# Performance work log

Hardware: AMD Instinct MI355X
Metric: run time of the kernel (lower is better)

Reference implementation:

```python
import jax, jax.numpy as jnp
import numpy as np

H = W = 240

def setup_inputs() -> dict:
    key = jax.random.key(0)
    k1, k2, k3 = jax.random.split(key, 3)
    B = 256
    T2_Gen = jax.random.normal(k1, (B, 1, H, W), dtype=jnp.float32)
    underT2_K = jax.random.normal(k2, (B, 2, H, W), dtype=jnp.float32)
    # k-space sampling mask (soft in [0,1); original uses a fixed undersampling mask)
    A = jax.random.uniform(k3, (H, W), dtype=jnp.float32)
    return {"T2_Gen": T2_Gen, "underT2_K": underT2_K, "A": A}

def reference(T2_Gen, underT2_K, A):
    # x2: [B, H, W]
    x2 = T2_Gen.reshape(-1, H, W)
    # batched 2D FFT over the last two axes (replaces the per-slice numpy loop)
    x2_k = jnp.fft.fft2(x2)  # complex64
    # undersampled k-space as complex: real = channel 0, imag = channel 1
    y_k = underT2_K[:, 0, :, :] + 1j * underT2_K[:, 1, :, :]
    z_k = (1.0 - A) * x2_k + y_k
    z = jnp.abs(jnp.fft.ifft2(z_k))  # [B, H, W] real
    return z.reshape(-1, 1, H, W)
```

## Files before the change

### kernel.cpp

```cpp
#include <hip/hip_runtime.h>
#include <math.h>

#define HW 240
#define PITCH 241
#define IMG_PIX (HW*HW)

__device__ __forceinline__ float2 cmul(float2 a, float2 b){
    return make_float2(a.x*b.x - a.y*b.y, a.x*b.y + a.y*b.x);
}
__device__ __forceinline__ float2 cadd(float2 a, float2 b){
    return make_float2(a.x+b.x, a.y+b.y);
}
__device__ __forceinline__ float2 csub(float2 a, float2 b){
    return make_float2(a.x-b.x, a.y-b.y);
}

template<int SIGN>
__device__ __forceinline__ void dft15(const float2* x, float2* X){
    const float S = (float)SIGN;
    const float s3 = 0.8660254037844387f;
    float2 y[5][3];
    #pragma unroll
    for (int n2 = 0; n2 < 5; ++n2){
        float2 a0 = x[n2], a1 = x[5+n2], a2 = x[10+n2];
        float2 t = cadd(a1, a2);
        float2 u = csub(a1, a2);
        float2 m = make_float2(a0.x - 0.5f*t.x, a0.y - 0.5f*t.y);
        float sx = S * s3;
        float2 s = make_float2(-sx*u.y, sx*u.x);
        y[n2][0] = cadd(a0, t);
        y[n2][1] = cadd(m, s);
        y[n2][2] = csub(m, s);
    }
    const float C15[9] = {1.f, 0.9135454576426009f, 0.6691306063588582f, 0.30901699437494745f,
                          -0.10452846326765346f, -0.5f, -0.8090169943749475f,
                          -0.9781476007338057f, -0.9781476007338057f};
    const float S15[9] = {0.f, 0.4067366430758004f, 0.7431448254773942f, 0.9510565162951535f,
                          0.9945218953682733f, 0.8660254037844387f, 0.5877852522924731f,
                          0.20791169081775931f, -0.20791169081775931f};
    #pragma unroll
    for (int n2 = 1; n2 < 5; ++n2){
        #pragma unroll
        for (int k1 = 1; k1 < 3; ++k1){
            const int e = n2*k1;
            y[n2][k1] = cmul(y[n2][k1], make_float2(C15[e], S*S15[e]));
        }
    }
    const float c1 = 0.30901699437494745f, s1 = 0.9510565162951535f;
    const float c2 = -0.8090169943749475f, s2 = 0.5877852522924731f;
    #pragma unroll
    for (int k1 = 0; k1 < 3; ++k1){
        float2 x0 = y[0][k1], x1 = y[1][k1], x2 = y[2][k1], x3 = y[3][k1], x4 = y[4][k1];
        float2 t1 = cadd(x1, x4), t3 = csub(x1, x4);
        float2 t2 = cadd(x2, x3), t4 = csub(x2, x3);
        X[k1] = make_float2(x0.x + t1.x + t2.x, x0.y + t1.y + t2.y);
        float2 u1 = make_float2(x0.x + c1*t1.x + c2*t2.x, x0.y + c1*t1.y + c2*t2.y);
        float2 u2 = make_float2(x0.x + c2*t1.x + c1*t2.x, x0.y + c2*t1.y + c1*t2.y);
        float2 v1 = make_float2(S*(s1*t3.x + s2*t4.x), S*(s1*t3.y + s2*t4.y));
        float2 v2 = make_float2(S*(s2*t3.x - s1*t4.x), S*(s2*t3.y - s1*t4.y));
        X[k1+3]  = make_float2(u1.x - v1.y, u1.y + v1.x);
        X[k1+12] = make_float2(u1.x + v1.y, u1.y - v1.x);
        X[k1+6]  = make_float2(u2.x - v2.y, u2.y + v2.x);
        X[k1+9]  = make_float2(u2.x + v2.y, u2.y - v2.x);
    }
}

template<int SIGN>
__device__ __forceinline__ void dft16(const float2* x, float2* X){
    const float S = (float)SIGN;
    float2 y[4][4];
    #pragma unroll
    for (int n2 = 0; n2 < 4; ++n2){
        float2 a0 = x[n2], a1 = x[4+n2], a2 = x[8+n2], a3 = x[12+n2];
        float2 t0 = cadd(a0,a2), t1 = csub(a0,a2);
        float2 t2 = cadd(a1,a3), t3 = csub(a1,a3);
        float2 it3 = make_float2(-S*t3.y, S*t3.x);
        y[n2][0] = cadd(t0,t2);
        y[n2][2] = csub(t0,t2);
        y[n2][1] = cadd(t1,it3);
        y[n2][3] = csub(t1,it3);
    }
    const float C16[10] = {1.f, 0.9238795325112867f, 0.7071067811865476f, 0.3826834323650898f,
                           0.f, -0.3826834323650898f, -0.7071067811865476f, -0.9238795325112867f,
                           -1.f, -0.9238795325112867f};
    const float S16[10] = {0.f, 0.3826834323650898f, 0.7071067811865476f, 0.9238795325112867f,
                           1.f, 0.9238795325112867f, 0.7071067811865476f, 0.3826834323650898f,
                           0.f, -0.3826834323650898f};
    #pragma unroll
    for (int n2 = 1; n2 < 4; ++n2){
        #pragma unroll
        for (int k1 = 1; k1 < 4; ++k1){
            const int e = n2*k1;
            y[n2][k1] = cmul(y[n2][k1], make_float2(C16[e], S*S16[e]));
        }
    }
    #pragma unroll
    for (int k1 = 0; k1 < 4; ++k1){
        float2 a0 = y[0][k1], a1 = y[1][k1], a2 = y[2][k1], a3 = y[3][k1];
        float2 t0 = cadd(a0,a2), t1 = csub(a0,a2);
        float2 t2 = cadd(a1,a3), t3 = csub(a1,a3);
        float2 it3 = make_float2(-S*t3.y, S*t3.x);
        X[k1]    = cadd(t0,t2);
        X[k1+8]  = csub(t0,t2);
        X[k1+4]  = cadd(t1,it3);
        X[k1+12] = csub(t1,it3);
    }
}

template<int SIGN>
__device__ void fft240(float2 (*sm)[PITCH], float2* v, int rl, int b){
    const float TWOPI = 6.28318530717958647692f;
    float2 Y[15];
    dft15<SIGN>(v, Y);
    float2 step, tw = make_float2(1.0f, 0.0f);
    {
        float ang = (float)SIGN * TWOPI * (float)b * (1.0f/240.0f);
        __sincosf(ang, &step.y, &step.x);
    }
    #pragma unroll
    for (int d = 0; d < 15; ++d){
        sm[rl][b*15 + d] = cmul(Y[d], tw);
        tw = cmul(tw, step);
    }
    __syncthreads();

    float2 Z[16];
    if (b < 15){
        #pragma unroll
        for (int bb = 0; bb < 16; ++bb) Z[bb] = sm[rl][bb*15 + b];
    }
    __syncthreads();
    if (b < 15){
        float2 XX[16];
        dft16<SIGN>(Z, XX);
        #pragma unroll
        for (int m = 0; m < 16; ++m) sm[rl][15*m + b] = XX[m];
    }
    __syncthreads();
}

__global__ __launch_bounds__(256) void passA_rowfft(const float* __restrict__ x,
                                                    float2* __restrict__ out){
    __shared__ float2 sm[16][PITCH];
    int g = blockIdx.x, img = g / 15, row0 = (g % 15) * 16;
    int tid = threadIdx.x, rl = tid >> 4, b = tid & 15;
    const float* src = x + (size_t)img * IMG_PIX + (size_t)(row0 + rl) * HW + b;
    float2 v[15];
    #pragma unroll
    for (int a = 0; a < 15; ++a) v[a] = make_float2(src[16*a], 0.0f);
    fft240<-1>(sm, v, rl, b);
    float2* dst = out + (size_t)img * IMG_PIX;
    #pragma unroll
    for (int j = 0; j < 15; ++j){
        int k  = j*16 + rl;
        dst[(size_t)k * HW + row0 + b] = sm[b][k];
    }
}

__global__ __launch_bounds__(256) void passB_col_dc_icol(const float2* __restrict__ in,
                                                         const float* __restrict__ under,
                                                         const float* __restrict__ Am,
                                                         float2* __restrict__ out){
    __shared__ float2 sm[16][PITCH];
    int g = blockIdx.x, img = g / 15, row0 = (g % 15) * 16;
    int tid = threadIdx.x, rl = tid >> 4, b = tid & 15;
    const float2* src = in + (size_t)img * IMG_PIX + (size_t)(row0 + rl) * HW + b;
    float2 v[15];
    #pragma unroll
    for (int a = 0; a < 15; ++a) v[a] = src[16*a];
    fft240<-1>(sm, v, rl, b);

    const float* y0 = under + (size_t)img * (2*IMG_PIX);
    const float* y1 = y0 + IMG_PIX;
    #pragma unroll
    for (int j = 0; j < 15; ++j){
        int kh = j*16 + rl;
        size_t p = (size_t)kh * HW + row0 + b;
        float s = 1.0f - Am[p];
        float2 X = sm[b][kh];
        sm[b][kh] = make_float2(s * X.x + y0[p], s * X.y + y1[p]);
    }
    __syncthreads();
    #pragma unroll
    for (int a = 0; a < 15; ++a) v[a] = sm[rl][16*a + b];
    __syncthreads();
    fft240<+1>(sm, v, rl, b);

    float2* dst = out + (size_t)img * IMG_PIX;
    #pragma unroll
    for (int j = 0; j < 15; ++j){
        int h = j*16 + rl;
        dst[(size_t)h * HW + row0 + b] = sm[b][h];
    }
}

__global__ __launch_bounds__(256) void passC_irow_abs(const float2* __restrict__ in,
                                                      float* __restrict__ out){
    __shared__ float2 sm[16][PITCH];
    int g = blockIdx.x, img = g / 15, row0 = (g % 15) * 16;
    int tid = threadIdx.x, rl = tid >> 4, b = tid & 15;
    const float2* src = in + (size_t)img * IMG_PIX + (size_t)(row0 + rl) * HW + b;
    float2 v[15];
    #pragma unroll
    for (int a = 0; a < 15; ++a) v[a] = src[16*a];
    fft240<+1>(sm, v, rl, b);
    float* dst = out + (size_t)img * IMG_PIX;
    const float scale = 1.0f / (float)IMG_PIX;
    #pragma unroll
    for (int j = 0; j < 15; ++j){
        int w = j*16 + b;
        float2 X = sm[rl][w];
        dst[(size_t)(row0 + rl) * HW + w] = sqrtf(X.x*X.x + X.y*X.y) * scale;
    }
}

extern "C" void kernel_launch(void* const* d_in, const int* in_sizes, int n_in,
                              void* d_out, int out_size, void* d_ws, size_t ws_size,
                              hipStream_t stream){
    const float* T2   = (const float*)d_in[0];
    const float* U    = (const float*)d_in[1];
    const float* Am   = (const float*)d_in[2];
    float* out        = (float*)d_out;

    const int B = 256;
    float2* s1 = (float2*)d_ws;
    float2* s2 = s1 + (size_t)B * IMG_PIX;

    dim3 grid(B * 15), block(256);
    passA_rowfft     <<<grid, block, 0, stream>>>(T2, s1);
    passB_col_dc_icol<<<grid, block, 0, stream>>>(s1, U, Am, s2);
    passC_irow_abs   <<<grid, block, 0, stream>>>(s2, out);
}
```

Before: 313.4 us.

## Store FFT intermediates as half2 in tiled layout with coalesced staging

The complex intermediates between the three FFT passes are now stored as fp16 half2 instead of float2, which halves intermediate global traffic. They are written in a column-tile-major layout so each block reads and writes one contiguous tile, and global loads and stores go through shared memory to stay coalesced. Normalization is split into a 1/240 factor applied after the column pass and again at the end, which keeps fp16 values in range. The risk is accuracy loss from fp16 rounding of FFT values, plus extra shared-memory staging and barriers.

Measured after the change: 283.6 us. 9.5% less time.

```diff
diff --git a/kernel.cpp b/kernel.cpp
--- a/kernel.cpp
+++ b/kernel.cpp
@@ -1,9 +1,12 @@
 #include <hip/hip_runtime.h>
+#include <hip/hip_fp16.h>
 #include <math.h>
 
 #define HW 240
 #define PITCH 241
 #define IMG_PIX (HW*HW)
+#define NB 15
+#define TILE_ELEMS (240*16)
 
 __device__ __forceinline__ float2 cmul(float2 a, float2 b){
     return make_float2(a.x*b.x - a.y*b.y, a.x*b.y + a.y*b.x);
@@ -14,6 +17,8 @@
 __device__ __forceinline__ float2 csub(float2 a, float2 b){
     return make_float2(a.x-b.x, a.y-b.y);
 }
+__device__ __forceinline__ __half2 f2h(float2 a){ return __floats2half2_rn(a.x, a.y); }
+__device__ __forceinline__ float2 h2f(__half2 h){ return make_float2(__low2float(h), __high2float(h)); }
 
 template<int SIGN>
 __device__ __forceinline__ void dft15(const float2* x, float2* X){
@@ -140,34 +145,49 @@
 }
 
 __global__ __launch_bounds__(256) void passA_rowfft(const float* __restrict__ x,
-                                                    float2* __restrict__ out){
+                                                    __half2* __restrict__ out){
     __shared__ float2 sm[16][PITCH];
-    int g = blockIdx.x, img = g / 15, row0 = (g % 15) * 16;
+    float* smf = (float*)sm;
+    int g = blockIdx.x, img = g / NB, h0 = (g % NB) * 16;
     int tid = threadIdx.x, rl = tid >> 4, b = tid & 15;
-    const float* src = x + (size_t)img * IMG_PIX + (size_t)(row0 + rl) * HW + b;
+    const float* src = x + (size_t)img * IMG_PIX + (size_t)h0 * HW;
+    #pragma unroll
+    for (int j = 0; j < 15; ++j){
+        int f = j*256 + tid;
+        smf[(f/HW)*(2*PITCH) + (f%HW)] = src[f];
+    }
+    __syncthreads();
     float2 v[15];
     #pragma unroll
-    for (int a = 0; a < 15; ++a) v[a] = make_float2(src[16*a], 0.0f);
+    for (int a = 0; a < 15; ++a) v[a] = make_float2(smf[rl*(2*PITCH) + 16*a + b], 0.0f);
+    __syncthreads();
     fft240<-1>(sm, v, rl, b);
-    float2* dst = out + (size_t)img * IMG_PIX;
-    #pragma unroll
-    for (int j = 0; j < 15; ++j){
-        int k  = j*16 + rl;
-        dst[(size_t)k * HW + row0 + b] = sm[b][k];
-    }
-}
-
-__global__ __launch_bounds__(256) void passB_col_dc_icol(const float2* __restrict__ in,
+    int hl = rl, kwin = b;
+    #pragma unroll
+    for (int kb = 0; kb < NB; ++kb){
+        float2 val = sm[hl][kb*16 + kwin];
+        out[((size_t)(img*NB + kb)*HW + h0 + hl)*16 + kwin] = f2h(val);
+    }
+}
+
+__global__ __launch_bounds__(256) void passB_col_dc_icol(const __half2* __restrict__ in,
                                                          const float* __restrict__ under,
                                                          const float* __restrict__ Am,
-                                                         float2* __restrict__ out){
+                                                         __half2* __restrict__ out){
     __shared__ float2 sm[16][PITCH];
-    int g = blockIdx.x, img = g / 15, row0 = (g % 15) * 16;
+    int g = blockIdx.x, img = g / NB, s = g % NB, kw0 = s * 16;
     int tid = threadIdx.x, rl = tid >> 4, b = tid & 15;
-    const float2* src = in + (size_t)img * IMG_PIX + (size_t)(row0 + rl) * HW + b;
+    const __half2* src = in + (size_t)(img*NB + s) * TILE_ELEMS;
+    #pragma unroll
+    for (int j = 0; j < 15; ++j){
+        int f = j*256 + tid;
+        sm[f & 15][f >> 4] = h2f(src[f]);
+    }
+    __syncthreads();
     float2 v[15];
     #pragma unroll
-    for (int a = 0; a < 15; ++a) v[a] = src[16*a];
+    for (int a = 0; a < 15; ++a) v[a] = sm[rl][16*a + b];
+    __syncthreads();
     fft240<-1>(sm, v, rl, b);
 
     const float* y0 = under + (size_t)img * (2*IMG_PIX);
@@ -175,10 +195,10 @@
     #pragma unroll
     for (int j = 0; j < 15; ++j){
         int kh = j*16 + rl;
-        size_t p = (size_t)kh * HW + row0 + b;
-        float s = 1.0f - Am[p];
+        size_t p = (size_t)kh * HW + kw0 + b;
+        float sc = 1.0f - Am[p];
         float2 X = sm[b][kh];
-        sm[b][kh] = make_float2(s * X.x + y0[p], s * X.y + y1[p]);
+        sm[b][kh] = make_float2(sc * X.x + y0[p], sc * X.y + y1[p]);
     }
     __syncthreads();
     #pragma unroll
@@ -186,31 +206,41 @@
     __syncthreads();
     fft240<+1>(sm, v, rl, b);
 
-    float2* dst = out + (size_t)img * IMG_PIX;
-    #pragma unroll
-    for (int j = 0; j < 15; ++j){
-        int h = j*16 + rl;
-        dst[(size_t)h * HW + row0 + b] = sm[b][h];
-    }
-}
-
-__global__ __launch_bounds__(256) void passC_irow_abs(const float2* __restrict__ in,
-                                                      float* __restrict__ out){
+    const float inv240 = 1.0f / 240.0f;
+    __half2* dst = out + (size_t)(img*NB + s) * TILE_ELEMS;
+    #pragma unroll
+    for (int j = 0; j < 15; ++j){
+        int f = j*256 + tid;
+        float2 val = sm[f & 15][f >> 4];
+        val.x *= inv240; val.y *= inv240;
+        dst[f] = f2h(val);
+    }
+}
+
+__global__ __launch_bounds__(256) void passC_irow_abs(const __half2* __restrict__ in,
+                                                      float* __restrict__ outp){
     __shared__ float2 sm[16][PITCH];
-    int g = blockIdx.x, img = g / 15, row0 = (g % 15) * 16;
+    int g = blockIdx.x, img = g / NB, h0 = (g % NB) * 16;
     int tid = threadIdx.x, rl = tid >> 4, b = tid & 15;
-    const float2* src = in + (size_t)img * IMG_PIX + (size_t)(row0 + rl) * HW + b;
+    int hl = rl, kwin = b;
+    #pragma unroll
+    for (int kb = 0; kb < NB; ++kb){
+        __half2 hv = in[((size_t)(img*NB + kb)*HW + h0 + hl)*16 + kwin];
+        sm[hl][kb*16 + kwin] = h2f(hv);
+    }
+    __syncthreads();
     float2 v[15];
     #pragma unroll
-    for (int a = 0; a < 15; ++a) v[a] = src[16*a];
+    for (int a = 0; a < 15; ++a) v[a] = sm[rl][16*a + b];
+    __syncthreads();
     fft240<+1>(sm, v, rl, b);
-    float* dst = out + (size_t)img * IMG_PIX;
-    const float scale = 1.0f / (float)IMG_PIX;
-    #pragma unroll
-    for (int j = 0; j < 15; ++j){
-        int w = j*16 + b;
-        float2 X = sm[rl][w];
-        dst[(size_t)(row0 + rl) * HW + w] = sqrtf(X.x*X.x + X.y*X.y) * scale;
+    float* dst = outp + (size_t)img * IMG_PIX + (size_t)h0 * HW;
+    const float inv240 = 1.0f / 240.0f;
+    #pragma unroll
+    for (int j = 0; j < 15; ++j){
+        int f = j*256 + tid;
+        float2 X = sm[f/HW][f%HW];
+        dst[f] = sqrtf(X.x*X.x + X.y*X.y) * inv240;
     }
 }
 
@@ -223,11 +253,11 @@
     float* out        = (float*)d_out;
 
     const int B = 256;
-    float2* s1 = (float2*)d_ws;
-    float2* s2 = s1 + (size_t)B * IMG_PIX;
-
-    dim3 grid(B * 15), block(256);
-    passA_rowfft     <<<grid, block, 0, stream>>>(T2, s1);
-    passB_col_dc_icol<<<grid, block, 0, stream>>>(s1, U, Am, s2);
-    passC_irow_abs   <<<grid, block, 0, stream>>>(s2, out);
-}
+    __half2* i1 = (__half2*)d_ws;
+    __half2* i2 = i1 + (size_t)B * IMG_PIX;
+
+    dim3 grid(B * NB), block(256);
+    passA_rowfft     <<<grid, block, 0, stream>>>(T2, i1);
+    passB_col_dc_icol<<<grid, block, 0, stream>>>(i1, U, Am, i2);
+    passC_irow_abs   <<<grid, block, 0, stream>>>(i2, out);
+}
```
